# Kernel optimization log

Hardware: AMD Instinct MI355X
Metric: run time of the kernel (lower is better)

Reference implementation:

```python
import jax, jax.numpy as jnp
import numpy as np
import math

N_NODES = 20000
N_EDGES = 320000
DIM = 256
NUM_HEADS = 8


def setup_inputs() -> dict:
    key = jax.random.key(0)
    ks = jax.random.split(key, 8)
    x = jax.random.normal(ks[0], (N_NODES, DIM), dtype=jnp.float32)
    edge_index = jax.random.randint(ks[1], (2, N_EDGES), 0, N_NODES, dtype=jnp.int64)
    edge_attr = jax.random.normal(ks[2], (N_EDGES, DIM), dtype=jnp.float32)
    s = 1.0 / math.sqrt(DIM)
    Wq = jax.random.uniform(ks[3], (DIM, DIM), jnp.float32, -s, s)
    Wk = jax.random.uniform(ks[4], (DIM, DIM), jnp.float32, -s, s)
    Wv = jax.random.uniform(ks[5], (DIM, DIM), jnp.float32, -s, s)
    We = jax.random.uniform(ks[6], (DIM, DIM), jnp.float32, -s, s)
    be = jax.random.uniform(ks[7], (DIM,), jnp.float32, -s, s)
    return {"x": x, "edge_index": edge_index, "edge_attr": edge_attr,
            "Wq": Wq, "Wk": Wk, "Wv": Wv, "We": We, "be": be}


def reference(x, edge_index, edge_attr, Wq, Wk, Wv, We, be):
    N = x.shape[0]
    E = edge_attr.shape[0]
    H = NUM_HEADS
    C = DIM // H  # per-head channels (concat=True)
    src = edge_index[0]  # segment / attention-grouping index
    dst = edge_index[1]
    # Z = edge_attr * x[dst]  -> [E, D]
    Z = edge_attr * x[dst]
    q = x @ Wq.T          # [N, D]
    k = Z @ Wk.T          # [E, D]
    v = Z @ Wv.T          # [E, D]
    edge_out = Z @ We.T + be  # [E, D]
    # split heads
    qh = q.reshape(N, H, C)
    kh = k.reshape(E, H, C)
    vh = v.reshape(E, H, C)
    # per-edge, per-head score: sum(q[src]*k)/sqrt(C)   -> [E, H]
    scores = jnp.einsum('ehc,ehc->eh', qh[src], kh) / math.sqrt(C)
    # segment softmax grouped by src node
    m = jax.ops.segment_max(scores, src, num_segments=N)        # [N, H]
    ex = jnp.exp(scores - m[src])                               # [E, H]
    denom = jax.ops.segment_sum(ex, src, num_segments=N)        # [N, H]
    attn = ex / (denom[src] + 1e-16)                            # [E, H]
    # weighted scatter-sum of values -> [N, H, C] -> [N, D]
    out = jax.ops.segment_sum(attn[:, :, None] * vh, src, num_segments=N)
    out = out.reshape(N, H * C)
    return (out, edge_out)
```

## Files before the change

### kernel.cpp

```cpp
#include <hip/hip_runtime.h>
#include <math.h>

#define NN 20000
#define NE 320000
#define DIM 256

typedef __bf16 bf16x8 __attribute__((ext_vector_type(8)));
typedef float f32x4 __attribute__((ext_vector_type(4)));
typedef int i32x4 __attribute__((ext_vector_type(4)));
typedef unsigned short u16x4 __attribute__((ext_vector_type(4)));

union B8 { i32x4 i; bf16x8 b; };

__device__ __forceinline__ unsigned short f2bf(float f) {
  unsigned int u; __builtin_memcpy(&u, &f, 4);
  u += 0x7fffu + ((u >> 16) & 1u);
  return (unsigned short)(u >> 16);
}
__device__ __forceinline__ float bf2f(unsigned short h) {
  unsigned int u = ((unsigned int)h) << 16;
  float f; __builtin_memcpy(&f, &u, 4);
  return f;
}

__global__ __launch_bounds__(256) void pack_w(const float* __restrict__ W,
                                              unsigned short* __restrict__ wf) {
  int t = blockIdx.x * 256 + threadIdx.x;
  int lane = t & 63, ct = (t >> 6) & 15, ks = t >> 10;
  int col = ct * 16 + (lane & 15);
  int k0 = ks * 32 + (lane >> 4) * 8;
  const float* src = W + col * 256 + k0;
  unsigned int h[8];
#pragma unroll
  for (int j = 0; j < 8; j++) h[j] = f2bf(src[j]);
  i32x4 v;
  v.x = (int)(h[0] | (h[1] << 16));
  v.y = (int)(h[2] | (h[3] << 16));
  v.z = (int)(h[4] | (h[5] << 16));
  v.w = (int)(h[6] | (h[7] << 16));
  ((i32x4*)wf)[t] = v;
}

__device__ __forceinline__ void gemm_tile(const unsigned short* zs,
                                          const unsigned short* wf,
                                          int lane, int wv, f32x4 (&acc)[4][4]) {
#pragma unroll 1
  for (int ksI = 0; ksI < 8; ksI++) {
    bf16x8 afr[4], bfr[4];
#pragma unroll
    for (int rt = 0; rt < 4; rt++) {
      int row = rt * 16 + (lane & 15);
      int k = ksI * 32 + (lane >> 4) * 8;
      int byteo = (row * 512 + k * 2) ^ ((row & 7) << 4);
      B8 u; u.i = *(const i32x4*)((const char*)zs + byteo);
      afr[rt] = u.b;
    }
#pragma unroll
    for (int ct = 0; ct < 4; ct++) {
      B8 u; u.i = ((const i32x4*)wf)[ksI * 1024 + (wv * 4 + ct) * 64 + lane];
      bfr[ct] = u.b;
    }
#pragma unroll
    for (int rt = 0; rt < 4; rt++)
#pragma unroll
      for (int ct = 0; ct < 4; ct++)
        acc[rt][ct] = __builtin_amdgcn_mfma_f32_16x16x32_bf16(afr[rt], bfr[ct], acc[rt][ct], 0, 0, 0);
  }
}

__global__ __launch_bounds__(256) void q_kernel(const float* __restrict__ x,
                                                const unsigned short* __restrict__ wf,
                                                float* __restrict__ q) {
  __shared__ unsigned short zs[64 * 256];
  int tid = threadIdx.x, lane = tid & 63, wv = tid >> 6;
  int r0 = blockIdx.x * 64;
  int dcol = lane * 4;
#pragma unroll 4
  for (int rr = 0; rr < 16; rr++) {
    int r = rr * 4 + wv;
    int row = r0 + r;
    f32x4 a = {0.f, 0.f, 0.f, 0.f};
    if (row < NN) a = *(const f32x4*)(x + (size_t)row * DIM + dcol);
    u16x4 z;
    z.x = f2bf(a.x); z.y = f2bf(a.y); z.z = f2bf(a.z); z.w = f2bf(a.w);
    int byteo = (r * 512 + dcol * 2) ^ ((r & 7) << 4);
    *(u16x4*)((char*)zs + byteo) = z;
  }
  __syncthreads();
  f32x4 acc[4][4];
#pragma unroll
  for (int rt = 0; rt < 4; rt++)
#pragma unroll
    for (int ct = 0; ct < 4; ct++) acc[rt][ct] = (f32x4){0.f, 0.f, 0.f, 0.f};
  gemm_tile(zs, wf, lane, wv, acc);
  int cq = lane & 15, rq = lane >> 4;
#pragma unroll
  for (int ct = 0; ct < 4; ct++) {
    int col = wv * 64 + ct * 16 + cq;
#pragma unroll
    for (int rt = 0; rt < 4; rt++) {
#pragma unroll
      for (int j = 0; j < 4; j++) {
        int row = r0 + rt * 16 + rq * 4 + j;
        if (row < NN) q[(size_t)row * DIM + col] = acc[rt][ct][j];
      }
    }
  }
}

__global__ __launch_bounds__(256) void edge_kernel(
    const float* __restrict__ x, const int* __restrict__ ei,
    const float* __restrict__ ea,
    const unsigned short* __restrict__ wfk, const unsigned short* __restrict__ wfv,
    const unsigned short* __restrict__ wfe, const float* __restrict__ be,
    const float* __restrict__ q, unsigned short* __restrict__ vws,
    float* __restrict__ scores, float* __restrict__ edge_out) {
  __shared__ unsigned short zs[64 * 256];
  __shared__ int dsts[64], srcs[64];
  int tid = threadIdx.x, lane = tid & 63, wv = tid >> 6;
  int e0 = blockIdx.x * 64;
  if (tid < 64) {
    srcs[tid] = ei[e0 + tid];
    dsts[tid] = ei[NE + e0 + tid];
  }
  __syncthreads();
  int dcol = lane * 4;
#pragma unroll 4
  for (int rr = 0; rr < 16; rr++) {
    int r = rr * 4 + wv;
    f32x4 a = *(const f32x4*)(ea + (size_t)(e0 + r) * DIM + dcol);
    f32x4 b = *(const f32x4*)(x + (size_t)dsts[r] * DIM + dcol);
    u16x4 z;
    z.x = f2bf(a.x * b.x); z.y = f2bf(a.y * b.y);
    z.z = f2bf(a.z * b.z); z.w = f2bf(a.w * b.w);
    int byteo = (r * 512 + dcol * 2) ^ ((r & 7) << 4);
    *(u16x4*)((char*)zs + byteo) = z;
  }
  __syncthreads();
  int cq = lane & 15, rq = lane >> 4;
#pragma unroll 1
  for (int w3 = 0; w3 < 3; w3++) {
    const unsigned short* wf = (w3 == 0) ? wfv : (w3 == 1) ? wfe : wfk;
    f32x4 acc[4][4];
#pragma unroll
    for (int rt = 0; rt < 4; rt++)
#pragma unroll
      for (int ct = 0; ct < 4; ct++) acc[rt][ct] = (f32x4){0.f, 0.f, 0.f, 0.f};
    gemm_tile(zs, wf, lane, wv, acc);
    if (w3 == 0) {
#pragma unroll
      for (int ct = 0; ct < 4; ct++) {
        int col = wv * 64 + ct * 16 + cq;
#pragma unroll
        for (int rt = 0; rt < 4; rt++)
#pragma unroll
          for (int j = 0; j < 4; j++) {
            int row = rt * 16 + rq * 4 + j;
            vws[(size_t)(e0 + row) * DIM + col] = f2bf(acc[rt][ct][j]);
          }
      }
    } else if (w3 == 1) {
#pragma unroll
      for (int ct = 0; ct < 4; ct++) {
        int col = wv * 64 + ct * 16 + cq;
        float bias = be[col];
#pragma unroll
        for (int rt = 0; rt < 4; rt++)
#pragma unroll
          for (int j = 0; j < 4; j++) {
            int row = rt * 16 + rq * 4 + j;
            edge_out[(size_t)(e0 + row) * DIM + col] = acc[rt][ct][j] + bias;
          }
      }
    } else {
      __syncthreads();
#pragma unroll
      for (int ct = 0; ct < 4; ct++) {
        int col = wv * 64 + ct * 16 + cq;
#pragma unroll
        for (int rt = 0; rt < 4; rt++)
#pragma unroll
          for (int j = 0; j < 4; j++) {
            int row = rt * 16 + rq * 4 + j;
            zs[row * 256 + col] = f2bf(acc[rt][ct][j]);
          }
      }
      __syncthreads();
#pragma unroll
      for (int s2 = 0; s2 < 2; s2++) {
        int sidx = s2 * 256 + tid;
        int r = sidx >> 3, h = sidx & 7;
        const unsigned short* kp = zs + r * 256 + h * 32;
        const float* qp = q + (size_t)srcs[r] * DIM + h * 32;
        float acs = 0.f;
#pragma unroll
        for (int c8 = 0; c8 < 4; c8++) {
          i32x4 kv = *(const i32x4*)(kp + c8 * 8);
          f32x4 qa = *(const f32x4*)(qp + c8 * 8);
          f32x4 qb = *(const f32x4*)(qp + c8 * 8 + 4);
          acs += bf2f((unsigned short)(kv.x & 0xffff)) * qa.x
               + bf2f((unsigned short)(kv.x >> 16)) * qa.y
               + bf2f((unsigned short)(kv.y & 0xffff)) * qa.z
               + bf2f((unsigned short)(kv.y >> 16)) * qa.w
               + bf2f((unsigned short)(kv.z & 0xffff)) * qb.x
               + bf2f((unsigned short)(kv.z >> 16)) * qb.y
               + bf2f((unsigned short)(kv.w & 0xffff)) * qb.z
               + bf2f((unsigned short)(kv.w >> 16)) * qb.w;
        }
        scores[(size_t)(e0 + r) * 8 + h] = acs * 0.17677669529663687f;
      }
    }
  }
}

__global__ __launch_bounds__(256) void count_kernel(const int* __restrict__ ei,
                                                    int* __restrict__ counts) {
  int e = blockIdx.x * 256 + threadIdx.x;
  if (e < NE) atomicAdd(&counts[ei[e]], 1);
}

__global__ __launch_bounds__(256) void scan_kernel(const int* __restrict__ counts,
                                                   int* __restrict__ offs,
                                                   int* __restrict__ cursor) {
  __shared__ int tmp[256];
  __shared__ int carry;
  int tid = threadIdx.x;
  if (tid == 0) carry = 0;
  __syncthreads();
  for (int base = 0; base < NN; base += 256) {
    int i = base + tid;
    int v = (i < NN) ? counts[i] : 0;
    tmp[tid] = v;
    __syncthreads();
    for (int off = 1; off < 256; off <<= 1) {
      int t = (tid >= off) ? tmp[tid - off] : 0;
      __syncthreads();
      tmp[tid] += t;
      __syncthreads();
    }
    int incl = tmp[tid];
    int c0 = carry;
    if (i < NN) {
      offs[i] = c0 + incl - v;
      cursor[i] = c0 + incl - v;
    }
    __syncthreads();
    if (tid == 255) carry = c0 + incl;
    __syncthreads();
  }
  if (tid == 0) offs[NN] = carry;
}

__global__ __launch_bounds__(256) void fill_kernel(const int* __restrict__ ei,
                                                   int* __restrict__ cursor,
                                                   int* __restrict__ eids) {
  int e = blockIdx.x * 256 + threadIdx.x;
  if (e < NE) {
    int pos = atomicAdd(&cursor[ei[e]], 1);
    eids[pos] = e;
  }
}

__global__ __launch_bounds__(256) void node_kernel(const int* __restrict__ offs,
                                                   const int* __restrict__ eids,
                                                   const float* __restrict__ scores,
                                                   const unsigned short* __restrict__ vws,
                                                   float* __restrict__ out) {
  int tid = threadIdx.x;
  int n = blockIdx.x * 4 + (tid >> 6);
  int lane = tid & 63, h = lane >> 3;
  int o0 = offs[n], deg = offs[n + 1] - o0;
  float m = -INFINITY, s = 0.f;
  float a0 = 0.f, a1 = 0.f, a2 = 0.f, a3 = 0.f;
  for (int i = 0; i < deg; i++) {
    int e = eids[o0 + i];
    float sc = scores[(size_t)e * 8 + h];
    float mn = fmaxf(m, sc);
    float scale = __expf(m - mn);
    float p = __expf(sc - mn);
    s = s * scale + p;
    m = mn;
    u16x4 v = *(const u16x4*)(vws + (size_t)e * DIM + lane * 4);
    a0 = a0 * scale + p * bf2f(v.x);
    a1 = a1 * scale + p * bf2f(v.y);
    a2 = a2 * scale + p * bf2f(v.z);
    a3 = a3 * scale + p * bf2f(v.w);
  }
  float inv = 1.f / (s + 1e-16f);
  f32x4 o;
  o.x = a0 * inv; o.y = a1 * inv; o.z = a2 * inv; o.w = a3 * inv;
  *(f32x4*)(out + (size_t)n * DIM + lane * 4) = o;
}

extern "C" void kernel_launch(void* const* d_in, const int* in_sizes, int n_in,
                              void* d_out, int out_size, void* d_ws, size_t ws_size,
                              hipStream_t stream) {
  const float* x = (const float*)d_in[0];
  const int* ei = (const int*)d_in[1];
  const float* ea = (const float*)d_in[2];
  const float* Wq = (const float*)d_in[3];
  const float* Wk = (const float*)d_in[4];
  const float* Wv = (const float*)d_in[5];
  const float* We = (const float*)d_in[6];
  const float* be = (const float*)d_in[7];

  float* out = (float*)d_out;
  float* edge_out = out + (size_t)NN * DIM;
  float* q = out;
  char* ws = (char*)d_ws;
  unsigned short* wfq = (unsigned short*)(ws + 0);
  unsigned short* wfk = (unsigned short*)(ws + 131072);
  unsigned short* wfv = (unsigned short*)(ws + 262144);
  unsigned short* wfe = (unsigned short*)(ws + 393216);
  unsigned short* vws = (unsigned short*)(ws + 524288);
  float* scores = (float*)(ws + 524288 + 163840000);
  int* counts = (int*)(ws + 524288 + 163840000 + 10240000);
  int* offs = (int*)(ws + 524288 + 163840000 + 10240000 + 80000);
  int* cursor = (int*)(ws + 524288 + 163840000 + 10240000 + 160016);
  int* eids = (int*)(ws + 524288 + 163840000 + 10240000 + 240016);

  hipMemsetAsync(counts, 0, NN * sizeof(int), stream);

  pack_w<<<32, 256, 0, stream>>>(Wq, wfq);
  pack_w<<<32, 256, 0, stream>>>(Wk, wfk);
  pack_w<<<32, 256, 0, stream>>>(Wv, wfv);
  pack_w<<<32, 256, 0, stream>>>(We, wfe);

  q_kernel<<<(NN + 63) / 64, 256, 0, stream>>>(x, wfq, q);
  edge_kernel<<<NE / 64, 256, 0, stream>>>(x, ei, ea, wfk, wfv, wfe, be, q,
                                           vws, scores, edge_out);

  count_kernel<<<(NE + 255) / 256, 256, 0, stream>>>(ei, counts);
  scan_kernel<<<1, 256, 0, stream>>>(counts, offs, cursor);
  fill_kernel<<<(NE + 255) / 256, 256, 0, stream>>>(ei, cursor, eids);

  node_kernel<<<NN / 4, 256, 0, stream>>>(offs, eids, scores, vws, out);
}
```

Measured before the change: 759.2 us.

## Restructure edge kernel into 128-edge tiles with pipelined swapped-operand MFMA passes

```diff
diff --git a/kernel.cpp b/kernel.cpp
--- a/kernel.cpp
+++ b/kernel.cpp
@@ -108,109 +108,130 @@
   }
 }
 
-__global__ __launch_bounds__(256) void edge_kernel(
+__global__ __launch_bounds__(512) void edge_kernel(
     const float* __restrict__ x, const int* __restrict__ ei,
     const float* __restrict__ ea,
     const unsigned short* __restrict__ wfk, const unsigned short* __restrict__ wfv,
     const unsigned short* __restrict__ wfe, const float* __restrict__ be,
     const float* __restrict__ q, unsigned short* __restrict__ vws,
     float* __restrict__ scores, float* __restrict__ edge_out) {
-  __shared__ unsigned short zs[64 * 256];
-  __shared__ int dsts[64], srcs[64];
+  __shared__ unsigned short zs[128 * 256];
   int tid = threadIdx.x, lane = tid & 63, wv = tid >> 6;
-  int e0 = blockIdx.x * 64;
-  if (tid < 64) {
-    srcs[tid] = ei[e0 + tid];
-    dsts[tid] = ei[NE + e0 + tid];
-  }
-  __syncthreads();
-  int dcol = lane * 4;
-#pragma unroll 4
-  for (int rr = 0; rr < 16; rr++) {
-    int r = rr * 4 + wv;
-    f32x4 a = *(const f32x4*)(ea + (size_t)(e0 + r) * DIM + dcol);
-    f32x4 b = *(const f32x4*)(x + (size_t)dsts[r] * DIM + dcol);
+  int wm = wv >> 2, wn = wv & 3;
+  int rq = lane >> 4, cl = lane & 15;
+  int e0 = blockIdx.x * 128;
+
+#pragma unroll
+  for (int i = 0; i < 16; i++) {
+    int r = i * 8 + wv;
+    int dst = ei[NE + e0 + r];
+    f32x4 a = *(const f32x4*)(ea + (size_t)(e0 + r) * DIM + lane * 4);
+    f32x4 b = *(const f32x4*)(x + (size_t)dst * DIM + lane * 4);
     u16x4 z;
     z.x = f2bf(a.x * b.x); z.y = f2bf(a.y * b.y);
     z.z = f2bf(a.z * b.z); z.w = f2bf(a.w * b.w);
-    int byteo = (r * 512 + dcol * 2) ^ ((r & 7) << 4);
+    int byteo = (r * 512 + lane * 8) ^ ((r & 7) << 4);
     *(u16x4*)((char*)zs + byteo) = z;
   }
   __syncthreads();
-  int cq = lane & 15, rq = lane >> 4;
-#pragma unroll 1
-  for (int w3 = 0; w3 < 3; w3++) {
-    const unsigned short* wf = (w3 == 0) ? wfv : (w3 == 1) ? wfe : wfk;
-    f32x4 acc[4][4];
-#pragma unroll
-    for (int rt = 0; rt < 4; rt++)
-#pragma unroll
-      for (int ct = 0; ct < 4; ct++) acc[rt][ct] = (f32x4){0.f, 0.f, 0.f, 0.f};
-    gemm_tile(zs, wf, lane, wv, acc);
-    if (w3 == 0) {
-#pragma unroll
-      for (int ct = 0; ct < 4; ct++) {
-        int col = wv * 64 + ct * 16 + cq;
-#pragma unroll
-        for (int rt = 0; rt < 4; rt++)
-#pragma unroll
-          for (int j = 0; j < 4; j++) {
-            int row = rt * 16 + rq * 4 + j;
-            vws[(size_t)(e0 + row) * DIM + col] = f2bf(acc[rt][ct][j]);
-          }
-      }
-    } else if (w3 == 1) {
-#pragma unroll
-      for (int ct = 0; ct < 4; ct++) {
-        int col = wv * 64 + ct * 16 + cq;
-        float bias = be[col];
-#pragma unroll
-        for (int rt = 0; rt < 4; rt++)
-#pragma unroll
-          for (int j = 0; j < 4; j++) {
-            int row = rt * 16 + rq * 4 + j;
-            edge_out[(size_t)(e0 + row) * DIM + col] = acc[rt][ct][j] + bias;
-          }
-      }
-    } else {
-      __syncthreads();
-#pragma unroll
-      for (int ct = 0; ct < 4; ct++) {
-        int col = wv * 64 + ct * 16 + cq;
-#pragma unroll
-        for (int rt = 0; rt < 4; rt++)
-#pragma unroll
-          for (int j = 0; j < 4; j++) {
-            int row = rt * 16 + rq * 4 + j;
-            zs[row * 256 + col] = f2bf(acc[rt][ct][j]);
-          }
-      }
-      __syncthreads();
-#pragma unroll
-      for (int s2 = 0; s2 < 2; s2++) {
-        int sidx = s2 * 256 + tid;
-        int r = sidx >> 3, h = sidx & 7;
-        const unsigned short* kp = zs + r * 256 + h * 32;
-        const float* qp = q + (size_t)srcs[r] * DIM + h * 32;
-        float acs = 0.f;
-#pragma unroll
-        for (int c8 = 0; c8 < 4; c8++) {
-          i32x4 kv = *(const i32x4*)(kp + c8 * 8);
-          f32x4 qa = *(const f32x4*)(qp + c8 * 8);
-          f32x4 qb = *(const f32x4*)(qp + c8 * 8 + 4);
-          acs += bf2f((unsigned short)(kv.x & 0xffff)) * qa.x
-               + bf2f((unsigned short)(kv.x >> 16)) * qa.y
-               + bf2f((unsigned short)(kv.y & 0xffff)) * qa.z
-               + bf2f((unsigned short)(kv.y >> 16)) * qa.w
-               + bf2f((unsigned short)(kv.z & 0xffff)) * qb.x
-               + bf2f((unsigned short)(kv.z >> 16)) * qb.y
-               + bf2f((unsigned short)(kv.w & 0xffff)) * qb.z
-               + bf2f((unsigned short)(kv.w >> 16)) * qb.w;
-        }
-        scores[(size_t)(e0 + r) * 8 + h] = acs * 0.17677669529663687f;
-      }
-    }
-  }
+
+  const unsigned short* wfs[3] = {wfv, wfe, wfk};
+  i32x4 wbuf[4][4];
+  i32x4 zbuf[2][4];
+  f32x4 acc[4][4];
+
+#define LOADW(S, SLOT)                                                         \
+  {                                                                            \
+    const unsigned short* wfp = wfs[(S) >> 3];                                 \
+    _Pragma("unroll") for (int a = 0; a < 4; a++)                              \
+        wbuf[SLOT][a] =                                                        \
+            ((const i32x4*)wfp)[((S) & 7) * 1024 + (wn * 4 + a) * 64 + lane];  \
+  }
+#define LOADZ(S, SLOT)                                                         \
+  {                                                                            \
+    _Pragma("unroll") for (int b = 0; b < 4; b++) {                            \
+      int row = wm * 64 + b * 16 + cl;                                         \
+      int kk = ((S) & 7) * 32 + rq * 8;                                        \
+      int byteo = (row * 512 + kk * 2) ^ ((row & 7) << 4);                     \
+      zbuf[SLOT][b] = *(const i32x4*)((const char*)zs + byteo);                \
+    }                                                                          \
+  }
+#define GEMM_PASS(P)                                                           \
+  _Pragma("unroll") for (int a = 0; a < 4; a++)                                \
+      _Pragma("unroll") for (int b = 0; b < 4; b++)                            \
+          acc[a][b] = (f32x4){0.f, 0.f, 0.f, 0.f};                             \
+  _Pragma("unroll") for (int ks = 0; ks < 8; ks++) {                           \
+    const int step = (P) * 8 + ks;                                             \
+    if (step + 2 < 24) LOADW(step + 2, (step + 2) & 3);                        \
+    if (step + 1 < 24) LOADZ(step + 1, (step + 1) & 1);                        \
+    _Pragma("unroll") for (int a = 0; a < 4; a++) {                            \
+      B8 w; w.i = wbuf[step & 3][a];                                           \
+      _Pragma("unroll") for (int b = 0; b < 4; b++) {                          \
+        B8 z; z.i = zbuf[step & 1][b];                                         \
+        acc[a][b] = __builtin_amdgcn_mfma_f32_16x16x32_bf16(w.b, z.b,          \
+                                                            acc[a][b], 0, 0, 0); \
+      }                                                                        \
+    }                                                                          \
+  }
+
+  LOADW(0, 0); LOADW(1, 1);
+  LOADZ(0, 0); LOADZ(1, 1);
+
+  GEMM_PASS(0)
+#pragma unroll
+  for (int a = 0; a < 4; a++) {
+    int ch = wn * 64 + a * 16 + rq * 4;
+#pragma unroll
+    for (int b = 0; b < 4; b++) {
+      int edge = wm * 64 + b * 16 + cl;
+      u16x4 o;
+      o.x = f2bf(acc[a][b][0]); o.y = f2bf(acc[a][b][1]);
+      o.z = f2bf(acc[a][b][2]); o.w = f2bf(acc[a][b][3]);
+      *(u16x4*)(vws + (size_t)(e0 + edge) * DIM + ch) = o;
+    }
+  }
+
+  GEMM_PASS(1)
+#pragma unroll
+  for (int a = 0; a < 4; a++) {
+    int ch = wn * 64 + a * 16 + rq * 4;
+    f32x4 bias = *(const f32x4*)(be + ch);
+#pragma unroll
+    for (int b = 0; b < 4; b++) {
+      int edge = wm * 64 + b * 16 + cl;
+      f32x4 o = acc[a][b] + bias;
+      *(f32x4*)(edge_out + (size_t)(e0 + edge) * DIM + ch) = o;
+    }
+  }
+
+  GEMM_PASS(2)
+#pragma unroll
+  for (int b = 0; b < 4; b++) {
+    int edge = wm * 64 + b * 16 + cl;
+    int sr = ei[e0 + edge];
+    const float* qp = q + (size_t)sr * DIM + wn * 64 + rq * 4;
+    f32x4 q0 = *(const f32x4*)(qp);
+    f32x4 q1 = *(const f32x4*)(qp + 16);
+    f32x4 q2 = *(const f32x4*)(qp + 32);
+    f32x4 q3 = *(const f32x4*)(qp + 48);
+    float s0 = acc[0][b][0] * q0[0] + acc[0][b][1] * q0[1] +
+               acc[0][b][2] * q0[2] + acc[0][b][3] * q0[3] +
+               acc[1][b][0] * q1[0] + acc[1][b][1] * q1[1] +
+               acc[1][b][2] * q1[2] + acc[1][b][3] * q1[3];
+    float s1 = acc[2][b][0] * q2[0] + acc[2][b][1] * q2[1] +
+               acc[2][b][2] * q2[2] + acc[2][b][3] * q2[3] +
+               acc[3][b][0] * q3[0] + acc[3][b][1] * q3[1] +
+               acc[3][b][2] * q3[2] + acc[3][b][3] * q3[3];
+    s0 += __shfl_xor(s0, 16); s0 += __shfl_xor(s0, 32);
+    s1 += __shfl_xor(s1, 16); s1 += __shfl_xor(s1, 32);
+    if (lane < 16) {
+      scores[(size_t)(e0 + edge) * 8 + wn * 2 + 0] = s0 * 0.17677669529663687f;
+      scores[(size_t)(e0 + edge) * 8 + wn * 2 + 1] = s1 * 0.17677669529663687f;
+    }
+  }
+#undef LOADW
+#undef LOADZ
+#undef GEMM_PASS
 }
 
 __global__ __launch_bounds__(256) void count_kernel(const int* __restrict__ ei,
@@ -327,8 +348,8 @@
   pack_w<<<32, 256, 0, stream>>>(We, wfe);
 
   q_kernel<<<(NN + 63) / 64, 256, 0, stream>>>(x, wfq, q);
-  edge_kernel<<<NE / 64, 256, 0, stream>>>(x, ei, ea, wfk, wfv, wfe, be, q,
-                                           vws, scores, edge_out);
+  edge_kernel<<<NE / 128, 512, 0, stream>>>(x, ei, ea, wfk, wfv, wfe, be, q,
+                                            vws, scores, edge_out);
 
   count_kernel<<<(NE + 255) / 256, 256, 0, stream>>>(ei, counts);
   scan_kernel<<<1, 256, 0, stream>>>(counts, offs, cursor);
```

Measured after the change: 613.6 us. 19.2% less time.
